# Performance work log

Measured on AMD Instinct MI355X. Metric: run time of the kernel, lower is better.

## Reference

```python
import jax, jax.numpy as jnp
import numpy as np

N_PER_G = 100  # nodes per graph


def setup_inputs() -> dict:
    key = jax.random.key(0)
    ks = jax.random.split(key, 12)
    N, G, E = 100000, 1000, 1600000
    ninp, nout, K, H, H2 = 3, 10, 5, 64, 32
    x = jax.random.normal(ks[0], (N, ninp), jnp.float32)
    # within-graph random edges (contiguous node blocks per graph)
    epg = E // G
    gid = jnp.arange(E, dtype=jnp.int32) // epg
    src = jax.random.randint(ks[1], (E,), 0, N_PER_G, jnp.int32) + gid * N_PER_G
    dst = jax.random.randint(ks[2], (E,), 0, N_PER_G, jnp.int32) + gid * N_PER_G
    edge_index = jnp.stack([src, dst])
    batch = (jnp.arange(N, dtype=jnp.int32) // N_PER_G)
    lambda_max = 1.5 + 0.5 * jax.random.uniform(ks[3], (G,), jnp.float32)
    s = 0.05
    W1 = jax.random.normal(ks[4], (K, ninp, H), jnp.float32) * s
    b1 = jnp.zeros((H,), jnp.float32)
    W2 = jax.random.normal(ks[5], (K, H, H), jnp.float32) * s
    b2 = jnp.zeros((H,), jnp.float32)
    W3 = jax.random.normal(ks[6], (K, H, H), jnp.float32) * s
    b3 = jnp.zeros((H,), jnp.float32)
    bn_gamma = jnp.ones((H,), jnp.float32)
    bn_beta = jnp.zeros((H,), jnp.float32)
    bn_mean = jnp.zeros((H,), jnp.float32)
    bn_var = jnp.ones((H,), jnp.float32)
    fc1_w = jax.random.normal(ks[7], (H, H2), jnp.float32) * s
    fc1_b = jnp.zeros((H2,), jnp.float32)
    fc2_w = jax.random.normal(ks[8], (H2, nout), jnp.float32) * s
    fc2_b = jnp.zeros((nout,), jnp.float32)
    return dict(x=x, edge_index=edge_index, batch=batch, lambda_max=lambda_max,
                W1=W1, b1=b1, W2=W2, b2=b2, W3=W3, b3=b3,
                bn_gamma=bn_gamma, bn_beta=bn_beta, bn_mean=bn_mean, bn_var=bn_var,
                fc1_w=fc1_w, fc1_b=fc1_b, fc2_w=fc2_w, fc2_b=fc2_b)


def _cheb_conv(x, W, b, row, col, coef_edge, coef_loop):
    # PyG ChebConv with sym-normalized scaled Laplacian:
    # Lhat x = scatter_add(coef_edge * x[col] -> row) + coef_loop * x
    N = x.shape[0]
    def lhat(h):
        return jax.ops.segment_sum(coef_edge[:, None] * h[col], row,
                                   num_segments=N) + coef_loop[:, None] * h
    Tx0 = x
    out = Tx0 @ W[0]
    Tx1 = lhat(x)
    out = out + Tx1 @ W[1]
    for k in range(2, W.shape[0]):
        Tx2 = 2.0 * lhat(Tx1) - Tx0
        out = out + Tx2 @ W[k]
        Tx0, Tx1 = Tx1, Tx2
    return out + b


def reference(x, edge_index, batch, lambda_max,
              W1, b1, W2, b2, W3, b3,
              bn_gamma, bn_beta, bn_mean, bn_var,
              fc1_w, fc1_b, fc2_w, fc2_b):
    N = x.shape[0]
    G = lambda_max.shape[0]
    row, col = edge_index[0], edge_index[1]
    # sym Laplacian normalization, scaled by 2/lambda_max (per-graph)
    deg = jax.ops.segment_sum(jnp.ones_like(row, dtype=x.dtype), row, num_segments=N)
    dis = jnp.where(deg > 0, deg, 1.0) ** -0.5
    dis = jnp.where(deg > 0, dis, 0.0)
    lmax_e = lambda_max[batch[row]]
    coef_edge = -(2.0 / lmax_e) * dis[row] * dis[col]   # off-diagonal of Lhat
    coef_loop = 2.0 / lambda_max[batch] - 1.0           # diagonal of Lhat
    h = jax.nn.relu(_cheb_conv(x, W1, b1, row, col, coef_edge, coef_loop))
    h = jax.nn.relu(_cheb_conv(h, W2, b2, row, col, coef_edge, coef_loop))
    h = jax.nn.relu(_cheb_conv(h, W3, b3, row, col, coef_edge, coef_loop))
    # global mean pool over graphs
    sums = jax.ops.segment_sum(h, batch, num_segments=G)
    cnts = jax.ops.segment_sum(jnp.ones((N,), h.dtype), batch, num_segments=G)
    g = sums / jnp.maximum(cnts, 1.0)[:, None]
    # BatchNorm1d (eval mode, running stats), eps=1e-5
    g = (g - bn_mean) * jax.lax.rsqrt(bn_var + 1e-5) * bn_gamma + bn_beta
    g = jax.nn.relu(g @ fc1_w + fc1_b)
    return jax.nn.log_softmax(g @ fc2_w + fc2_b, axis=1)
```

## Files before the change

### kernel.cpp

```cpp
#include <hip/hip_runtime.h>

#define NPG 100
#define HF 64
#define ST 72
#define SAT 136
#define CMW 29

typedef float  f4   __attribute__((ext_vector_type(4)));
typedef float  f16v __attribute__((ext_vector_type(16)));
typedef short  bf8  __attribute__((ext_vector_type(8)));

#define SZ_TC   (HF * SAT * 2)
#define SZ_TRM  (128 * ST * 2)
#define OFF_TC1  SZ_TC
#define OFF_TRM0 (2 * SZ_TC)
#define OFF_MISC (OFF_TRM0 + 2 * SZ_TRM)
#define SMEM_BYTES (OFF_MISC + 1280)
#define CMBYTES (128 * CMW * 4)

#define WT_TOTAL 46080

__device__ __forceinline__ unsigned short f2bf(float f) {
    unsigned u = __float_as_uint(f);
    u += 0x7fffu + ((u >> 16) & 1u);
    return (unsigned short)(u >> 16);
}
__device__ __forceinline__ unsigned cvt_pk_bf16(float lo, float hi) {
    unsigned r;
    asm("v_cvt_pk_bf16_f32 %0, %1, %2" : "=v"(r) : "v"(lo), "v"(hi));
    return r;
}
__device__ __forceinline__ f16v zerov16() {
    f16v z;
    #pragma unroll
    for (int i = 0; i < 16; i++) z[i] = 0.f;
    return z;
}
__device__ __forceinline__ void bar_lgkm() {
    asm volatile("s_waitcnt lgkmcnt(0)" ::: "memory");
    __builtin_amdgcn_s_barrier();
    __builtin_amdgcn_sched_barrier(0);
}
__device__ __forceinline__ void wait_lgkm() {
    asm volatile("s_waitcnt lgkmcnt(0)" ::: "memory");
}

union BF8U { unsigned u[4]; bf8 b; };

__global__ void wconv(const float* __restrict__ W1, const float* __restrict__ W2,
                      const float* __restrict__ W3, unsigned short* __restrict__ ws)
{
    int idx = blockIdx.x * 256 + threadIdx.x;
    if (idx >= WT_TOTAL) return;
    float v;
    if (idx < 5120) {
        int k5 = idx >> 10, rem = idx & 1023, fo = rem >> 4, fi = rem & 15;
        v = (fi < 3) ? W1[(k5 * 3 + fi) * HF + fo] : 0.f;
    } else if (idx < 25600) {
        int j = idx - 5120;
        int k5 = j >> 12, rem = j & 4095, fo = rem >> 6, fi = rem & 63;
        v = W2[(k5 * HF + fi) * HF + fo];
    } else {
        int j = idx - 25600;
        int k5 = j >> 12, rem = j & 4095, fo = rem >> 6, fi = rem & 63;
        v = W3[(k5 * HF + fi) * HF + fo];
    }
    ws[idx] = f2bf(v);
}

__launch_bounds__(256, 2)
__global__ void chebreg(const float* __restrict__ x, const int* __restrict__ ei,
                        const float* __restrict__ lambda_max,
                        const unsigned short* __restrict__ Wt,
                        const float* __restrict__ b1, const float* __restrict__ b2,
                        const float* __restrict__ b3,
                        const float* __restrict__ bng, const float* __restrict__ bnb,
                        const float* __restrict__ bnm, const float* __restrict__ bnv,
                        const float* __restrict__ fc1w, const float* __restrict__ fc1b,
                        const float* __restrict__ fc2w, const float* __restrict__ fc2b,
                        float* __restrict__ out, int E_total, int epg)
{
    extern __shared__ char sm[];
    const int tid = threadIdx.x;
    const int g = blockIdx.x;
    const int ebase = g * epg, nbase = g * NPG;
    const int wg = tid >> 6, lane = tid & 63;
    const int l31 = lane & 31, hh = lane >> 5;
    const int ht  = wg & 1;
    const int Mt0 = (wg >> 1) * 2;
    const int fo  = ht * 32 + l31;

    unsigned* Cm   = (unsigned*)(sm + OFF_TC1);
    unsigned* deg  = (unsigned*)(sm + OFF_MISC);
    float* pool    = (float*)(sm + OFF_MISC + 448);
    float* gvn     = (float*)(sm + OFF_MISC + 704);
    float* zf      = (float*)(sm + OFF_MISC + 960);
    float* logits  = (float*)(sm + OFF_MISC + 1088);
    float* lsep    = (float*)(sm + OFF_MISC + 1152);

    const float lam = lambda_max[g];
    const float two_l = 2.0f / lam;
    const float cl = two_l - 1.0f;

    float xr0 = 0.f, xr1 = 0.f, xr2 = 0.f;
    const bool tv = (tid < NPG);
    if (tv) {
        xr0 = x[(nbase + tid) * 3 + 0];
        xr1 = x[(nbase + tid) * 3 + 1];
        xr2 = x[(nbase + tid) * 3 + 2];
    }

    for (int i = tid; i < SZ_TC / 16; i += 256)
        ((f4*)sm)[i] = (f4){0.f, 0.f, 0.f, 0.f};
    for (int i = tid; i < CMBYTES / 16; i += 256)
        ((f4*)(sm + OFF_TC1))[i] = (f4){0.f, 0.f, 0.f, 0.f};
    for (int i = tid; i < SZ_TRM / 16; i += 256)
        ((f4*)(sm + OFF_TRM0))[i] = (f4){0.f, 0.f, 0.f, 0.f};
    if (tid < 112) deg[tid] = 0u;
    if (tid < HF) pool[tid] = 0.f;
    bar_lgkm();

    for (int e = tid; e < epg; e += 256) {
        int r = ei[ebase + e] - nbase;
        int c = ei[E_total + ebase + e] - nbase;
        atomicAdd(&Cm[r * CMW + (c >> 2)], 1u << (8 * (c & 3)));
        atomicAdd(&deg[r], 1u);
    }
    if (tv) {
        unsigned short h0 = f2bf(xr0);
        unsigned short h1 = f2bf(xr1);
        unsigned short h2 = f2bf(xr2);
        *(unsigned*)(sm + OFF_TRM0 + (tid * ST) * 2) = (unsigned)h0 | ((unsigned)h1 << 16);
        *(unsigned short*)(sm + OFF_TRM0 + (tid * ST + 2) * 2) = h2;
        *(unsigned short*)(sm + (0 * SAT + tid) * 2) = h0;
        *(unsigned short*)(sm + (1 * SAT + tid) * 2) = h1;
        *(unsigned short*)(sm + (2 * SAT + tid) * 2) = h2;
    }
    bar_lgkm();

    bf8 af[2][7];
    {
        int rr[2]; bool rv[2]; float base[2];
        #pragma unroll
        for (int m = 0; m < 2; m++) {
            rr[m] = 32 * (Mt0 + m) + l31;
            rv[m] = (rr[m] < NPG);
            unsigned dgr = rv[m] ? deg[rr[m]] : 0u;
            float disr = dgr ? rsqrtf((float)dgr) : 0.f;
            base[m] = rv[m] ? (-two_l * disr) : 0.f;
        }
        #pragma unroll
        for (int Ks = 0; Ks < 7; Ks++) {
            int k0 = Ks * 16 + 8 * hh;
            float dv8[8];
            #pragma unroll
            for (int j = 0; j < 8; j++) {
                unsigned dg = deg[k0 + j];
                dv8[j] = dg ? rsqrtf((float)dg) : 0.f;
            }
            #pragma unroll
            for (int m = 0; m < 2; m++) {
                unsigned w0 = rv[m] ? Cm[rr[m] * CMW + (k0 >> 2)]     : 0u;
                unsigned w1 = rv[m] ? Cm[rr[m] * CMW + (k0 >> 2) + 1] : 0u;
                float vv[8];
                #pragma unroll
                for (int j = 0; j < 8; j++) {
                    int k = k0 + j;
                    unsigned cnt = (((j < 4) ? w0 : w1) >> (8 * (k & 3))) & 255u;
                    float v = base[m] * (float)cnt * dv8[j];
                    if (rv[m] && k == rr[m]) v += cl;
                    vv[j] = v;
                }
                BF8U t;
                #pragma unroll
                for (int p = 0; p < 4; p++) t.u[p] = cvt_pk_bf16(vv[2 * p], vv[2 * p + 1]);
                af[m][Ks] = t.b;
            }
        }
    }
    bf8 bwp[4];
    bwp[0] = *(const bf8*)(Wt + fo * 16 + 8 * hh);
    bar_lgkm();

    f16v acc[2];
    unsigned prev[2][8], oldr[2][8];
    const float* bsv[3] = {b1, b2, b3};

    for (int L = 0; L < 3; L++) {
        const bool l1 = (L == 0);
        const unsigned short* Wl = l1 ? Wt : (Wt + (L == 1 ? 5120 : 25600));
        const int pb = L & 1;
        const int nKs = l1 ? 1 : 4;
        const float bias = bsv[L][fo];
        acc[0] = zerov16();
        acc[1] = zerov16();

        if (L == 0) {
            #pragma unroll
            for (int m = 0; m < 2; m++) {
                unsigned short tvv[16];
                #pragma unroll
                for (int r = 0; r < 16; r++) {
                    int np = (Mt0 + m) * 32 + (r & 3) + 8 * (r >> 2) + 4 * hh;
                    tvv[r] = *(const unsigned short*)(sm + OFF_TRM0 + (np * ST + fo) * 2);
                }
                #pragma unroll
                for (int p = 0; p < 8; p++)
                    prev[m][p] = (unsigned)tvv[2 * p] | ((unsigned)tvv[2 * p + 1] << 16);
            }
        }

        for (int s = 1; s <= 4; s++) {
            const int rp = (pb + s - 1) & 1, wp = rp ^ 1;
            const char* tcR = sm + rp * SZ_TC;
            const char* trR = sm + OFF_TRM0 + rp * SZ_TRM;
            char* tcW = sm + wp * SZ_TC;
            char* trW = sm + OFF_TRM0 + wp * SZ_TRM;

            #pragma unroll
            for (int Ks = 0; Ks < 4; Ks++) {
                if (Ks < nKs) {
                    #pragma unroll
                    for (int m = 0; m < 2; m++) {
                        bf8 a = *(const bf8*)(trR +
                                  (((Mt0 + m) * 32 + l31) * ST + Ks * 16 + 8 * hh) * 2);
                        acc[m] = __builtin_amdgcn_mfma_f32_32x32x16_bf16(a, bwp[Ks], acc[m], 0, 0, 0);
                    }
                }
            }
            if (l1) {
                bwp[0] = *(const bf8*)(Wl + (s * 64 + fo) * 16 + 8 * hh);
            } else {
                #pragma unroll
                for (int Ks = 0; Ks < 4; Ks++)
                    bwp[Ks] = *(const bf8*)(Wl + (s * 64 + fo) * 64 + Ks * 16 + 8 * hh);
            }

            bf8 bfr[7];
            #pragma unroll
            for (int Ks = 0; Ks < 7; Ks++)
                bfr[Ks] = *(const bf8*)(tcR + (fo * SAT + Ks * 16 + 8 * hh) * 2);

            #pragma unroll
            for (int m = 0; m < 2; m++) {
                f16v c = zerov16();
                #pragma unroll
                for (int Ks = 0; Ks < 7; Ks++)
                    c = __builtin_amdgcn_mfma_f32_32x32x16_bf16(af[m][Ks], bfr[Ks], c, 0, 0, 0);
                #pragma unroll
                for (int p = 0; p < 8; p++) {
                    float ve = c[2 * p], vo = c[2 * p + 1];
                    if (s >= 2) {
                        unsigned o = oldr[m][p];
                        ve = 2.f * ve - __uint_as_float(o << 16);
                        vo = 2.f * vo - __uint_as_float(o & 0xffff0000u);
                    }
                    oldr[m][p] = prev[m][p];
                    prev[m][p] = cvt_pk_bf16(ve, vo);
                }
                if (s < 4) {
                    #pragma unroll
                    for (int q4 = 0; q4 < 4; q4++) {
                        int np0 = (Mt0 + m) * 32 + 8 * q4 + 4 * hh;
                        uint2 pk;
                        pk.x = prev[m][2 * q4];
                        pk.y = prev[m][2 * q4 + 1];
                        *(uint2*)(tcW + (fo * SAT + np0) * 2) = pk;
                    }
                }
                #pragma unroll
                for (int p = 0; p < 8; p++) {
                    int r0 = 2 * p;
                    int npb = (Mt0 + m) * 32 + (r0 & 3) + 8 * (r0 >> 2) + 4 * hh;
                    char* ad = trW + (npb * ST + fo) * 2;
                    *(unsigned short*)ad = (unsigned short)prev[m][p];
                    *(unsigned short*)(ad + ST * 2) = (unsigned short)(prev[m][p] >> 16);
                }
            }
            bar_lgkm();
        }

        {
            const char* trR = sm + OFF_TRM0 + pb * SZ_TRM;
            #pragma unroll
            for (int Ks = 0; Ks < 4; Ks++) {
                if (Ks < nKs) {
                    #pragma unroll
                    for (int m = 0; m < 2; m++) {
                        bf8 a = *(const bf8*)(trR +
                                  (((Mt0 + m) * 32 + l31) * ST + Ks * 16 + 8 * hh) * 2);
                        acc[m] = __builtin_amdgcn_mfma_f32_32x32x16_bf16(a, bwp[Ks], acc[m], 0, 0, 0);
                    }
                }
            }
        }

        if (L < 2) {
            const unsigned short* Wn = Wt + (L == 0 ? 5120 : 25600);
            #pragma unroll
            for (int Ks = 0; Ks < 4; Ks++)
                bwp[Ks] = *(const bf8*)(Wn + fo * 64 + Ks * 16 + 8 * hh);

            const int op = pb ^ 1;
            char* tcW = sm + op * SZ_TC;
            char* trW = sm + OFF_TRM0 + op * SZ_TRM;
            #pragma unroll
            for (int m = 0; m < 2; m++) {
                #pragma unroll
                for (int p = 0; p < 8; p++) {
                    float ve = fmaxf(acc[m][2 * p]     + bias, 0.f);
                    float vo = fmaxf(acc[m][2 * p + 1] + bias, 0.f);
                    prev[m][p] = cvt_pk_bf16(ve, vo);
                }
                #pragma unroll
                for (int q4 = 0; q4 < 4; q4++) {
                    int np0 = (Mt0 + m) * 32 + 8 * q4 + 4 * hh;
                    uint2 pk;
                    pk.x = prev[m][2 * q4];
                    pk.y = prev[m][2 * q4 + 1];
                    *(uint2*)(tcW + (fo * SAT + np0) * 2) = pk;
                }
                #pragma unroll
                for (int p = 0; p < 8; p++) {
                    int r0 = 2 * p;
                    int npb = (Mt0 + m) * 32 + (r0 & 3) + 8 * (r0 >> 2) + 4 * hh;
                    char* ad = trW + (npb * ST + fo) * 2;
                    *(unsigned short*)ad = (unsigned short)prev[m][p];
                    *(unsigned short*)(ad + ST * 2) = (unsigned short)(prev[m][p] >> 16);
                }
            }
            bar_lgkm();
        } else {
            float ssum = 0.f;
            #pragma unroll
            for (int m = 0; m < 2; m++) {
                #pragma unroll
                for (int r = 0; r < 16; r++) {
                    int np = (Mt0 + m) * 32 + (r & 3) + 8 * (r >> 2) + 4 * hh;
                    float h = fmaxf(acc[m][r] + bias, 0.f);
                    if (np < NPG) ssum += h;
                }
            }
            ssum += __shfl_xor(ssum, 32, 64);
            if (hh == 0) atomicAdd(&pool[fo], ssum);
            bar_lgkm();
        }
    }

    if (wg == 0) {
        float gv = pool[lane] * (1.0f / NPG);
        gv = (gv - bnm[lane]) * rsqrtf(bnv[lane] + 1e-5f) * bng[lane] + bnb[lane];
        gvn[lane] = gv;
        wait_lgkm();
        if (lane < 32) {
            float a = fc1b[lane];
            for (int f = 0; f < HF; f++) a += gvn[f] * fc1w[f * 32 + lane];
            zf[lane] = fmaxf(a, 0.f);
        }
        wait_lgkm();
        if (lane < 10) {
            float a = fc2b[lane];
            for (int k = 0; k < 32; k++) a += zf[k] * fc2w[k * 10 + lane];
            logits[lane] = a;
        }
        wait_lgkm();
        if (lane == 0) {
            float m = logits[0];
            for (int i = 1; i < 10; i++) m = fmaxf(m, logits[i]);
            float s = 0.f;
            for (int i = 0; i < 10; i++) s += expf(logits[i] - m);
            lsep[0] = m + logf(s);
        }
        wait_lgkm();
        if (lane < 10) out[g * 10 + lane] = logits[lane] - lsep[0];
    }
}

extern "C" void kernel_launch(void* const* d_in, const int* in_sizes, int n_in,
                              void* d_out, int out_size, void* d_ws, size_t ws_size,
                              hipStream_t stream) {
    const float* x    = (const float*)d_in[0];
    const int*   ei   = (const int*)d_in[1];
    const float* lmax = (const float*)d_in[3];
    const float* W1   = (const float*)d_in[4];
    const float* b1   = (const float*)d_in[5];
    const float* W2   = (const float*)d_in[6];
    const float* b2   = (const float*)d_in[7];
    const float* W3   = (const float*)d_in[8];
    const float* b3   = (const float*)d_in[9];
    const float* bng  = (const float*)d_in[10];
    const float* bnb  = (const float*)d_in[11];
    const float* bnm  = (const float*)d_in[12];
    const float* bnv  = (const float*)d_in[13];
    const float* fc1w = (const float*)d_in[14];
    const float* fc1b = (const float*)d_in[15];
    const float* fc2w = (const float*)d_in[16];
    const float* fc2b = (const float*)d_in[17];

    const int E = in_sizes[1] / 2;
    const int G = in_sizes[3];
    const int epg = E / G;

    unsigned short* Wt = (unsigned short*)d_ws;

    wconv<<<(WT_TOTAL + 255) / 256, 256, 0, stream>>>(W1, W2, W3, Wt);

    hipFuncSetAttribute((const void*)chebreg,
                        hipFuncAttributeMaxDynamicSharedMemorySize, SMEM_BYTES);

    chebreg<<<G, 256, SMEM_BYTES, stream>>>(x, ei, lmax, Wt, b1, b2, b3,
                                            bng, bnb, bnm, bnv, fc1w, fc1b, fc2w, fc2b,
                                            (float*)d_out, E, epg);
}
```

Baseline: 157.5 us.

## Split row tiles across twice as many waves with 512-thread blocks

The block grows from 256 to 512 threads, so each wave now owns a single 32-row M tile instead of two. This halves the per-wave accumulators, the A-fragment registers and the MFMA chains. The intent is more wave-level parallelism and lower register pressure, which should improve latency hiding. In exchange the B fragments for the Laplacian product are loaded from LDS by twice as many waves, and each of the many barriers now has to synchronise more waves.

```diff
diff --git a/kernel.cpp b/kernel.cpp
--- a/kernel.cpp
+++ b/kernel.cpp
@@ -68,7 +68,7 @@
     ws[idx] = f2bf(v);
 }
 
-__launch_bounds__(256, 2)
+__launch_bounds__(512, 4)
 __global__ void chebreg(const float* __restrict__ x, const int* __restrict__ ei,
                         const float* __restrict__ lambda_max,
                         const unsigned short* __restrict__ Wt,
@@ -87,7 +87,7 @@
     const int wg = tid >> 6, lane = tid & 63;
     const int l31 = lane & 31, hh = lane >> 5;
     const int ht  = wg & 1;
-    const int Mt0 = (wg >> 1) * 2;
+    const int mt  = wg >> 1;
     const int fo  = ht * 32 + l31;
 
     unsigned* Cm   = (unsigned*)(sm + OFF_TC1);
@@ -110,17 +110,17 @@
         xr2 = x[(nbase + tid) * 3 + 2];
     }
 
-    for (int i = tid; i < SZ_TC / 16; i += 256)
+    for (int i = tid; i < SZ_TC / 16; i += 512)
         ((f4*)sm)[i] = (f4){0.f, 0.f, 0.f, 0.f};
-    for (int i = tid; i < CMBYTES / 16; i += 256)
+    for (int i = tid; i < CMBYTES / 16; i += 512)
         ((f4*)(sm + OFF_TC1))[i] = (f4){0.f, 0.f, 0.f, 0.f};
-    for (int i = tid; i < SZ_TRM / 16; i += 256)
+    for (int i = tid; i < SZ_TRM / 16; i += 512)
         ((f4*)(sm + OFF_TRM0))[i] = (f4){0.f, 0.f, 0.f, 0.f};
     if (tid < 112) deg[tid] = 0u;
     if (tid < HF) pool[tid] = 0.f;
     bar_lgkm();
 
-    for (int e = tid; e < epg; e += 256) {
+    for (int e = tid; e < epg; e += 512) {
         int r = ei[ebase + e] - nbase;
         int c = ei[E_total + ebase + e] - nbase;
         atomicAdd(&Cm[r * CMW + (c >> 2)], 1u << (8 * (c & 3)));
@@ -138,52 +138,41 @@
     }
     bar_lgkm();
 
-    bf8 af[2][7];
+    bf8 af[7];
     {
-        int rr[2]; bool rv[2]; float base[2];
-        #pragma unroll
-        for (int m = 0; m < 2; m++) {
-            rr[m] = 32 * (Mt0 + m) + l31;
-            rv[m] = (rr[m] < NPG);
-            unsigned dgr = rv[m] ? deg[rr[m]] : 0u;
-            float disr = dgr ? rsqrtf((float)dgr) : 0.f;
-            base[m] = rv[m] ? (-two_l * disr) : 0.f;
-        }
+        const int rr = 32 * mt + l31;
+        const bool rv = (rr < NPG);
+        unsigned dgr = rv ? deg[rr] : 0u;
+        float disr = dgr ? rsqrtf((float)dgr) : 0.f;
+        const float base = rv ? (-two_l * disr) : 0.f;
         #pragma unroll
         for (int Ks = 0; Ks < 7; Ks++) {
             int k0 = Ks * 16 + 8 * hh;
-            float dv8[8];
+            unsigned w0 = rv ? Cm[rr * CMW + (k0 >> 2)]     : 0u;
+            unsigned w1 = rv ? Cm[rr * CMW + (k0 >> 2) + 1] : 0u;
+            float vv[8];
             #pragma unroll
             for (int j = 0; j < 8; j++) {
-                unsigned dg = deg[k0 + j];
-                dv8[j] = dg ? rsqrtf((float)dg) : 0.f;
-            }
-            #pragma unroll
-            for (int m = 0; m < 2; m++) {
-                unsigned w0 = rv[m] ? Cm[rr[m] * CMW + (k0 >> 2)]     : 0u;
-                unsigned w1 = rv[m] ? Cm[rr[m] * CMW + (k0 >> 2) + 1] : 0u;
-                float vv[8];
-                #pragma unroll
-                for (int j = 0; j < 8; j++) {
-                    int k = k0 + j;
-                    unsigned cnt = (((j < 4) ? w0 : w1) >> (8 * (k & 3))) & 255u;
-                    float v = base[m] * (float)cnt * dv8[j];
-                    if (rv[m] && k == rr[m]) v += cl;
-                    vv[j] = v;
-                }
-                BF8U t;
-                #pragma unroll
-                for (int p = 0; p < 4; p++) t.u[p] = cvt_pk_bf16(vv[2 * p], vv[2 * p + 1]);
-                af[m][Ks] = t.b;
-            }
+                int k = k0 + j;
+                unsigned dg = deg[k];
+                float dv = dg ? rsqrtf((float)dg) : 0.f;
+                unsigned cnt = (((j < 4) ? w0 : w1) >> (8 * (k & 3))) & 255u;
+                float v = base * (float)cnt * dv;
+                if (rv && k == rr) v += cl;
+                vv[j] = v;
+            }
+            BF8U t;
+            #pragma unroll
+            for (int p = 0; p < 4; p++) t.u[p] = cvt_pk_bf16(vv[2 * p], vv[2 * p + 1]);
+            af[Ks] = t.b;
         }
     }
     bf8 bwp[4];
     bwp[0] = *(const bf8*)(Wt + fo * 16 + 8 * hh);
     bar_lgkm();
 
-    f16v acc[2];
-    unsigned prev[2][8], oldr[2][8];
+    f16v acc;
+    unsigned prev[8], oldr[8];
     const float* bsv[3] = {b1, b2, b3};
 
     for (int L = 0; L < 3; L++) {
@@ -192,22 +181,18 @@
         const int pb = L & 1;
         const int nKs = l1 ? 1 : 4;
         const float bias = bsv[L][fo];
-        acc[0] = zerov16();
-        acc[1] = zerov16();
+        acc = zerov16();
 
         if (L == 0) {
-            #pragma unroll
-            for (int m = 0; m < 2; m++) {
-                unsigned short tvv[16];
-                #pragma unroll
-                for (int r = 0; r < 16; r++) {
-                    int np = (Mt0 + m) * 32 + (r & 3) + 8 * (r >> 2) + 4 * hh;
-                    tvv[r] = *(const unsigned short*)(sm + OFF_TRM0 + (np * ST + fo) * 2);
-                }
-                #pragma unroll
-                for (int p = 0; p < 8; p++)
-                    prev[m][p] = (unsigned)tvv[2 * p] | ((unsigned)tvv[2 * p + 1] << 16);
-            }
+            unsigned short tvv[16];
+            #pragma unroll
+            for (int r = 0; r < 16; r++) {
+                int np = mt * 32 + (r & 3) + 8 * (r >> 2) + 4 * hh;
+                tvv[r] = *(const unsigned short*)(sm + OFF_TRM0 + (np * ST + fo) * 2);
+            }
+            #pragma unroll
+            for (int p = 0; p < 8; p++)
+                prev[p] = (unsigned)tvv[2 * p] | ((unsigned)tvv[2 * p + 1] << 16);
         }
 
         for (int s = 1; s <= 4; s++) {
@@ -220,12 +205,9 @@
             #pragma unroll
             for (int Ks = 0; Ks < 4; Ks++) {
                 if (Ks < nKs) {
-                    #pragma unroll
-                    for (int m = 0; m < 2; m++) {
-                        bf8 a = *(const bf8*)(trR +
-                                  (((Mt0 + m) * 32 + l31) * ST + Ks * 16 + 8 * hh) * 2);
-                        acc[m] = __builtin_amdgcn_mfma_f32_32x32x16_bf16(a, bwp[Ks], acc[m], 0, 0, 0);
-                    }
+                    bf8 a = *(const bf8*)(trR +
+                              ((mt * 32 + l31) * ST + Ks * 16 + 8 * hh) * 2);
+                    acc = __builtin_amdgcn_mfma_f32_32x32x16_bf16(a, bwp[Ks], acc, 0, 0, 0);
                 }
             }
             if (l1) {
@@ -236,46 +218,40 @@
                     bwp[Ks] = *(const bf8*)(Wl + (s * 64 + fo) * 64 + Ks * 16 + 8 * hh);
             }
 
-            bf8 bfr[7];
-            #pragma unroll
-            for (int Ks = 0; Ks < 7; Ks++)
-                bfr[Ks] = *(const bf8*)(tcR + (fo * SAT + Ks * 16 + 8 * hh) * 2);
-
-            #pragma unroll
-            for (int m = 0; m < 2; m++) {
-                f16v c = zerov16();
+            f16v c = zerov16();
+            #pragma unroll
+            for (int Ks = 0; Ks < 7; Ks++) {
+                bf8 bb = *(const bf8*)(tcR + (fo * SAT + Ks * 16 + 8 * hh) * 2);
+                c = __builtin_amdgcn_mfma_f32_32x32x16_bf16(af[Ks], bb, c, 0, 0, 0);
+            }
+            #pragma unroll
+            for (int p = 0; p < 8; p++) {
+                float ve = c[2 * p], vo = c[2 * p + 1];
+                if (s >= 2) {
+                    unsigned o = oldr[p];
+                    ve = 2.f * ve - __uint_as_float(o << 16);
+                    vo = 2.f * vo - __uint_as_float(o & 0xffff0000u);
+                }
+                oldr[p] = prev[p];
+                prev[p] = cvt_pk_bf16(ve, vo);
+            }
+            if (s < 4) {
                 #pragma unroll
-                for (int Ks = 0; Ks < 7; Ks++)
-                    c = __builtin_amdgcn_mfma_f32_32x32x16_bf16(af[m][Ks], bfr[Ks], c, 0, 0, 0);
-                #pragma unroll
-                for (int p = 0; p < 8; p++) {
-                    float ve = c[2 * p], vo = c[2 * p + 1];
-                    if (s >= 2) {
-                        unsigned o = oldr[m][p];
-                        ve = 2.f * ve - __uint_as_float(o << 16);
-                        vo = 2.f * vo - __uint_as_float(o & 0xffff0000u);
-                    }
-                    oldr[m][p] = prev[m][p];
-                    prev[m][p] = cvt_pk_bf16(ve, vo);
+                for (int q4 = 0; q4 < 4; q4++) {
+                    int np0 = mt * 32 + 8 * q4 + 4 * hh;
+                    uint2 pk;
+                    pk.x = prev[2 * q4];
+                    pk.y = prev[2 * q4 + 1];
+                    *(uint2*)(tcW + (fo * SAT + np0) * 2) = pk;
                 }
-                if (s < 4) {
-                    #pragma unroll
-                    for (int q4 = 0; q4 < 4; q4++) {
-                        int np0 = (Mt0 + m) * 32 + 8 * q4 + 4 * hh;
-                        uint2 pk;
-                        pk.x = prev[m][2 * q4];
-                        pk.y = prev[m][2 * q4 + 1];
-                        *(uint2*)(tcW + (fo * SAT + np0) * 2) = pk;
-                    }
-                }
-                #pragma unroll
-                for (int p = 0; p < 8; p++) {
-                    int r0 = 2 * p;
-                    int npb = (Mt0 + m) * 32 + (r0 & 3) + 8 * (r0 >> 2) + 4 * hh;
-                    char* ad = trW + (npb * ST + fo) * 2;
-                    *(unsigned short*)ad = (unsigned short)prev[m][p];
-                    *(unsigned short*)(ad + ST * 2) = (unsigned short)(prev[m][p] >> 16);
-                }
+            }
+            #pragma unroll
+            for (int p = 0; p < 8; p++) {
+                int r0 = 2 * p;
+                int npb = mt * 32 + (r0 & 3) + 8 * (r0 >> 2) + 4 * hh;
+                char* ad = trW + (npb * ST + fo) * 2;
+                *(unsigned short*)ad = (unsigned short)prev[p];
+                *(unsigned short*)(ad + ST * 2) = (unsigned short)(prev[p] >> 16);
             }
             bar_lgkm();
         }
@@ -285,12 +261,9 @@
             #pragma unroll
             for (int Ks = 0; Ks < 4; Ks++) {
                 if (Ks < nKs) {
-                    #pragma unroll
-                    for (int m = 0; m < 2; m++) {
-                        bf8 a = *(const bf8*)(trR +
-                                  (((Mt0 + m) * 32 + l31) * ST + Ks * 16 + 8 * hh) * 2);
-                        acc[m] = __builtin_amdgcn_mfma_f32_32x32x16_bf16(a, bwp[Ks], acc[m], 0, 0, 0);
-                    }
+                    bf8 a = *(const bf8*)(trR +
+                              ((mt * 32 + l31) * ST + Ks * 16 + 8 * hh) * 2);
+                    acc = __builtin_amdgcn_mfma_f32_32x32x16_bf16(a, bwp[Ks], acc, 0, 0, 0);
                 }
             }
         }
@@ -305,41 +278,35 @@
             char* tcW = sm + op * SZ_TC;
             char* trW = sm + OFF_TRM0 + op * SZ_TRM;
             #pragma unroll
-            for (int m = 0; m < 2; m++) {
-                #pragma unroll
-                for (int p = 0; p < 8; p++) {
-                    float ve = fmaxf(acc[m][2 * p]     + bias, 0.f);
-                    float vo = fmaxf(acc[m][2 * p + 1] + bias, 0.f);
-                    prev[m][p] = cvt_pk_bf16(ve, vo);
-                }
-                #pragma unroll
-                for (int q4 = 0; q4 < 4; q4++) {
-                    int np0 = (Mt0 + m) * 32 + 8 * q4 + 4 * hh;
-                    uint2 pk;
-                    pk.x = prev[m][2 * q4];
-                    pk.y = prev[m][2 * q4 + 1];
-                    *(uint2*)(tcW + (fo * SAT + np0) * 2) = pk;
-                }
-                #pragma unroll
-                for (int p = 0; p < 8; p++) {
-                    int r0 = 2 * p;
-                    int npb = (Mt0 + m) * 32 + (r0 & 3) + 8 * (r0 >> 2) + 4 * hh;
-                    char* ad = trW + (npb * ST + fo) * 2;
-                    *(unsigned short*)ad = (unsigned short)prev[m][p];
-                    *(unsigned short*)(ad + ST * 2) = (unsigned short)(prev[m][p] >> 16);
-                }
+            for (int p = 0; p < 8; p++) {
+                float ve = fmaxf(acc[2 * p]     + bias, 0.f);
+                float vo = fmaxf(acc[2 * p + 1] + bias, 0.f);
+                prev[p] = cvt_pk_bf16(ve, vo);
+            }
+            #pragma unroll
+            for (int q4 = 0; q4 < 4; q4++) {
+                int np0 = mt * 32 + 8 * q4 + 4 * hh;
+                uint2 pk;
+                pk.x = prev[2 * q4];
+                pk.y = prev[2 * q4 + 1];
+                *(uint2*)(tcW + (fo * SAT + np0) * 2) = pk;
+            }
+            #pragma unroll
+            for (int p = 0; p < 8; p++) {
+                int r0 = 2 * p;
+                int npb = mt * 32 + (r0 & 3) + 8 * (r0 >> 2) + 4 * hh;
+                char* ad = trW + (npb * ST + fo) * 2;
+                *(unsigned short*)ad = (unsigned short)prev[p];
+                *(unsigned short*)(ad + ST * 2) = (unsigned short)(prev[p] >> 16);
             }
             bar_lgkm();
         } else {
             float ssum = 0.f;
             #pragma unroll
-            for (int m = 0; m < 2; m++) {
-                #pragma unroll
-                for (int r = 0; r < 16; r++) {
-                    int np = (Mt0 + m) * 32 + (r & 3) + 8 * (r >> 2) + 4 * hh;
-                    float h = fmaxf(acc[m][r] + bias, 0.f);
-                    if (np < NPG) ssum += h;
-                }
+            for (int r = 0; r < 16; r++) {
+                int np = mt * 32 + (r & 3) + 8 * (r >> 2) + 4 * hh;
+                float h = fmaxf(acc[r] + bias, 0.f);
+                if (np < NPG) ssum += h;
             }
             ssum += __shfl_xor(ssum, 32, 64);
             if (hh == 0) atomicAdd(&pool[fo], ssum);
@@ -408,7 +375,7 @@
     hipFuncSetAttribute((const void*)chebreg,
                         hipFuncAttributeMaxDynamicSharedMemorySize, SMEM_BYTES);
 
-    chebreg<<<G, 256, SMEM_BYTES, stream>>>(x, ei, lmax, Wt, b1, b2, b3,
+    chebreg<<<G, 512, SMEM_BYTES, stream>>>(x, ei, lmax, Wt, b1, b2, b3,
                                             bng, bnb, bnm, bnv, fc1w, fc1b, fc2w, fc2b,
                                             (float*)d_out, E, epg);
 }
```

After: 157.5 us. About the same (+0.0%).
